# Kernel optimization log

Measured on AMD Instinct MI355X. Metric: run time of the kernel, lower is better.

Reference implementation:

```python
import jax, jax.numpy as jnp
import numpy as np

B, L, E, DK = 16, 2048, 1024, 128
MODE = "Decoder"


def setup_inputs() -> dict:
    key = jax.random.key(0)
    ks = jax.random.split(key, 6)
    x = jax.random.normal(ks[0], (B, L, E), dtype=jnp.float32)
    context = jax.random.normal(ks[1], (B, L, E), dtype=jnp.float32)
    batch_lengths = jax.random.randint(ks[2], (B,), 1, L + 1)  # valid lengths in [1, L]
    Wq = jax.random.normal(ks[3], (E, DK), dtype=jnp.float32) * 0.02
    Wk = jax.random.normal(ks[4], (E, DK), dtype=jnp.float32) * 0.02
    Wv = jax.random.normal(ks[5], (E, DK), dtype=jnp.float32) * 0.02
    return {"x": x, "context": context, "batch_lengths": batch_lengths,
            "Wq": Wq, "Wk": Wk, "Wv": Wv, "max_len": L}


def reference(x, context, batch_lengths, Wq, Wk, Wv, max_len):
    # x, context: [B, L, E]; batch_lengths: [B] ints; weights: [E, DK]
    Lq = x.shape[1]
    dk = Wq.shape[1]
    pos = jnp.arange(Lq)
    # outputMask: zero out padded time steps, broadcast over feature dim [B, L, 1]
    len_mask = (pos[None, :] < batch_lengths[:, None]).astype(x.dtype)[:, :, None]
    Q = (context @ Wq) * len_mask
    K = (context @ Wk) * len_mask
    V = (x @ Wv) * len_mask
    # energy: [B, Lq, Lk]
    energy = jnp.einsum("bqd,bkd->bqk", Q, K)
    # attnMask: -inf on padded key positions
    key_valid = pos[None, None, :] < batch_lengths[:, None, None]  # [B,1,Lk]
    if MODE == "Decoder":
        causal = pos[None, :, None] >= pos[None, None, :]  # j <= i
        key_valid = key_valid & causal
    energy = jnp.where(key_valid, energy, -jnp.inf)
    score = jax.nn.softmax(energy / jnp.sqrt(jnp.asarray(dk, x.dtype)), axis=-1)
    return jnp.einsum("bqk,bkd->bqd", score, V)
```

## Files before the change

### kernel.cpp

```cpp
#include <hip/hip_runtime.h>

#define DEV __device__ __forceinline__

typedef __attribute__((ext_vector_type(4))) float f32x4;
typedef __attribute__((ext_vector_type(4))) unsigned short u16x4;
typedef __attribute__((ext_vector_type(8))) __bf16 bf16x8;

constexpr int NB = 16, SL = 2048, EM = 1024, DKD = 128;

DEV unsigned short f2bf(float f) {
  unsigned int u = __float_as_uint(f);
  u += 0x7FFFu + ((u >> 16) & 1u);
  return (unsigned short)(u >> 16);
}

DEV f32x4 mfma16(bf16x8 a, bf16x8 b, f32x4 c) {
  return __builtin_amdgcn_mfma_f32_16x16x32_bf16(a, b, c, 0, 0, 0);
}

DEV void dma16(const void* g, void* l) {
  __builtin_amdgcn_global_load_lds(
      (const __attribute__((address_space(1))) unsigned int*)g,
      (__attribute__((address_space(3))) unsigned int*)l, 16, 0, 0);
}

DEV bf16x8 cvt8(f32x4 a, f32x4 b) {
  bf16x8 r;
  r[0] = (__bf16)a[0]; r[1] = (__bf16)a[1]; r[2] = (__bf16)a[2]; r[3] = (__bf16)a[3];
  r[4] = (__bf16)b[0]; r[5] = (__bf16)b[1]; r[6] = (__bf16)b[2]; r[7] = (__bf16)b[3];
  return r;
}

#define SBAR() __builtin_amdgcn_sched_barrier(0)

__global__ __launch_bounds__(256) void prep_w(
    const float* __restrict__ Wq, const float* __restrict__ Wk,
    const float* __restrict__ Wv, unsigned short* __restrict__ Wt,
    float* __restrict__ mvg)
{
  __shared__ unsigned short T[64 * 128];
  const int tid = threadIdx.x;
  if (blockIdx.x == 0) {
    #pragma unroll
    for (int i = 0; i < NB * DKD / 256; ++i) mvg[i * 256 + tid] = 0.f;
  }
  const int m = blockIdx.x >> 4, kc = blockIdx.x & 15;
  const float* W = (m == 0) ? Wq : ((m == 1) ? Wk : Wv);
  #pragma unroll
  for (int it = 0; it < 8; ++it) {
    int idx = it * 256 + tid;
    int kk = idx >> 5, n4 = (idx & 31) * 4;
    f32x4 w4 = *(const f32x4*)(W + (size_t)(kc * 64 + kk) * DKD + n4);
    *(u16x4*)&T[kk * 128 + n4] =
        u16x4{ f2bf(w4[0]), f2bf(w4[1]), f2bf(w4[2]), f2bf(w4[3]) };
  }
  __syncthreads();
  #pragma unroll
  for (int it = 0; it < 4; ++it) {
    int idx = it * 256 + tid;
    int p = idx & 7, n = idx >> 3;
    int c = p ^ (n & 7);
    unsigned short v[8];
    #pragma unroll
    for (int e = 0; e < 8; ++e) v[e] = T[(c * 8 + e) * 128 + n];
    size_t t = ((size_t)(m * 16 + kc) * 128 + n) * 8 + p;
    *(u16x4*)(Wt + t * 8)     = u16x4{v[0], v[1], v[2], v[3]};
    *(u16x4*)(Wt + t * 8 + 4) = u16x4{v[4], v[5], v[6], v[7]};
  }
}

__global__ __launch_bounds__(256, 2) void proj_qk(
    const float* __restrict__ ctx, const unsigned short* __restrict__ Wt,
    const int* __restrict__ lens, unsigned short* __restrict__ Qo,
    unsigned short* __restrict__ Kz)
{
  __shared__ float Als[2][64 * 64];
  const int tid = threadIdx.x;
  const int wave = tid >> 6, lane = tid & 63;
  const int quad = lane >> 4, mm = lane & 15;
  const int rb = blockIdx.x * 64;
  const int len = lens[blockIdx.x >> 5];
  if ((rb & (SL - 1)) >= len) return;

  f32x4 acc[4][4];
  #pragma unroll
  for (int i = 0; i < 4; ++i)
    #pragma unroll
    for (int j = 0; j < 4; ++j) acc[i][j] = f32x4{0.f, 0.f, 0.f, 0.f};

  const float* asrc[4];
  #pragma unroll
  for (int i = 0; i < 4; ++i) {
    const int rl_ = wave * 16 + i * 4 + (lane >> 4);
    const int cc  = (lane & 8) | ((lane & 7) ^ (rl_ & 7));
    asrc[i] = ctx + (size_t)(rb + rl_) * EM + cc * 4;
  }
  int soff[2][2];
  #pragma unroll
  for (int ks = 0; ks < 2; ++ks) {
    soff[ks][0] = (ks * 8 + ((quad * 2)     ^ (mm & 7))) * 4;
    soff[ks][1] = (ks * 8 + ((quad * 2 + 1) ^ (mm & 7))) * 4;
  }
  const unsigned short* bbase[4][2];
  #pragma unroll
  for (int lo = 0; lo < 4; ++lo)
    #pragma unroll
    for (int ks = 0; ks < 2; ++ks) {
      const int nrow = (wave * 4 + lo) * 16 + mm;
      const int pp = (ks * 4 + quad) ^ (mm & 7);
      const int cs = nrow * 8 + pp;
      bbase[lo][ks] = Wt + ((size_t)(cs >> 10) * 16384 + (cs & 1023)) * 8;
    }

  #pragma unroll
  for (int i = 0; i < 4; ++i)
    dma16(asrc[i],      (char*)Als[0] + wave * 4096 + i * 1024);
  #pragma unroll
  for (int i = 0; i < 4; ++i)
    dma16(asrc[i] + 64, (char*)Als[1] + wave * 4096 + i * 1024);
  __asm__ volatile("s_waitcnt vmcnt(4)" ::: "memory");
  __builtin_amdgcn_s_barrier();

  #pragma unroll 1
  for (int kc = 0; kc < 16; ++kc) {
    SBAR();
    bf16x8 bfr[4][2];
    #pragma unroll
    for (int lo = 0; lo < 4; ++lo)
      #pragma unroll
      for (int ks = 0; ks < 2; ++ks)
        bfr[lo][ks] = *(const bf16x8*)(bbase[lo][ks] + (size_t)kc * 8192);
    bf16x8 af[4][2];
    #pragma unroll
    for (int rt = 0; rt < 4; ++rt) {
      const float* rbase = Als[kc & 1] + (rt * 16 + mm) * 64;
      #pragma unroll
      for (int ks = 0; ks < 2; ++ks) {
        f32x4 a0 = *(const f32x4*)(rbase + soff[ks][0]);
        f32x4 a1 = *(const f32x4*)(rbase + soff[ks][1]);
        af[rt][ks] = cvt8(a0, a1);
      }
    }
    __asm__ volatile("s_waitcnt lgkmcnt(0)" ::: "memory");
    SBAR();
    __builtin_amdgcn_s_barrier();
    {
      const int kn = (kc + 2 < 16) ? (kc + 2) : 15;
      #pragma unroll
      for (int i = 0; i < 4; ++i)
        dma16(asrc[i] + kn * 64, (char*)Als[kc & 1] + wave * 4096 + i * 1024);
    }
    #pragma unroll
    for (int lo = 0; lo < 4; ++lo)
      #pragma unroll
      for (int ks = 0; ks < 2; ++ks)
        #pragma unroll
        for (int rt = 0; rt < 4; ++rt)
          acc[rt][lo] = mfma16(af[rt][ks], bfr[lo][ks], acc[rt][lo]);
    __builtin_amdgcn_s_barrier();
  }
  __asm__ volatile("s_waitcnt vmcnt(0)" ::: "memory");

  const float SCALE = 1.4426950408889634f * 0.08838834764831845f;
  #pragma unroll
  for (int rt = 0; rt < 4; ++rt)
    #pragma unroll
    for (int lo = 0; lo < 4; ++lo) {
      const int ctg = wave * 4 + lo;
      #pragma unroll
      for (int reg = 0; reg < 4; ++reg) {
        const int row = rb + rt * 16 + quad * 4 + reg;
        const int j = row & (SL - 1);
        const float val = acc[rt][lo][reg];
        if (ctg < 8) {
          const int d = ctg * 16 + mm;
          Qo[(size_t)row * DKD + d] = f2bf(val * ((j < len) ? SCALE : 0.f));
        } else {
          const int d = (ctg - 8) * 16 + mm;
          Kz[(size_t)row * DKD + (((d >> 3) ^ (j & 15)) * 8) + (d & 7)] = f2bf(val);
        }
      }
    }
}

__global__ __launch_bounds__(256, 2) void proj_v(
    const float* __restrict__ x, const unsigned short* __restrict__ Wt,
    const int* __restrict__ lens, unsigned short* __restrict__ Vz,
    float* __restrict__ mvg)
{
  __shared__ float Als[2][64 * 64];
  const int tid = threadIdx.x;
  const int wave = tid >> 6, lane = tid & 63;
  const int quad = lane >> 4, mm = lane & 15;
  const int rb = blockIdx.x * 64;
  const int bidx = blockIdx.x >> 5;
  const int len = lens[bidx];
  if ((rb & (SL - 1)) >= len) return;

  f32x4 acc[4][2];
  #pragma unroll
  for (int i = 0; i < 4; ++i) { acc[i][0] = f32x4{0.f,0.f,0.f,0.f}; acc[i][1] = f32x4{0.f,0.f,0.f,0.f}; }

  const float* asrc[4];
  #pragma unroll
  for (int i = 0; i < 4; ++i) {
    const int rl_ = wave * 16 + i * 4 + (lane >> 4);
    const int cc  = (lane & 8) | ((lane & 7) ^ (rl_ & 7));
    asrc[i] = x + (size_t)(rb + rl_) * EM + cc * 4;
  }
  int soff[2][2];
  #pragma unroll
  for (int ks = 0; ks < 2; ++ks) {
    soff[ks][0] = (ks * 8 + ((quad * 2)     ^ (mm & 7))) * 4;
    soff[ks][1] = (ks * 8 + ((quad * 2 + 1) ^ (mm & 7))) * 4;
  }
  const unsigned short* bbase[2][2];
  #pragma unroll
  for (int lo = 0; lo < 2; ++lo)
    #pragma unroll
    for (int ks = 0; ks < 2; ++ks) {
      const int nrow = (wave * 2 + lo) * 16 + mm;
      const int pp = (ks * 4 + quad) ^ (mm & 7);
      const int cs = nrow * 8 + pp;
      bbase[lo][ks] = Wt + ((size_t)2 * 16384 + cs) * 8;
    }

  #pragma unroll
  for (int i = 0; i < 4; ++i)
    dma16(asrc[i],      (char*)Als[0] + wave * 4096 + i * 1024);
  #pragma unroll
  for (int i = 0; i < 4; ++i)
    dma16(asrc[i] + 64, (char*)Als[1] + wave * 4096 + i * 1024);
  __asm__ volatile("s_waitcnt vmcnt(4)" ::: "memory");
  __builtin_amdgcn_s_barrier();

  #pragma unroll 1
  for (int kc = 0; kc < 16; ++kc) {
    SBAR();
    bf16x8 bfr[2][2];
    #pragma unroll
    for (int lo = 0; lo < 2; ++lo)
      #pragma unroll
      for (int ks = 0; ks < 2; ++ks)
        bfr[lo][ks] = *(const bf16x8*)(bbase[lo][ks] + (size_t)kc * 8192);
    bf16x8 af[4][2];
    #pragma unroll
    for (int rt = 0; rt < 4; ++rt) {
      const float* rbase = Als[kc & 1] + (rt * 16 + mm) * 64;
      #pragma unroll
      for (int ks = 0; ks < 2; ++ks) {
        f32x4 a0 = *(const f32x4*)(rbase + soff[ks][0]);
        f32x4 a1 = *(const f32x4*)(rbase + soff[ks][1]);
        af[rt][ks] = cvt8(a0, a1);
      }
    }
    __asm__ volatile("s_waitcnt lgkmcnt(0)" ::: "memory");
    SBAR();
    __builtin_amdgcn_s_barrier();
    {
      const int kn = (kc + 2 < 16) ? (kc + 2) : 15;
      #pragma unroll
      for (int i = 0; i < 4; ++i)
        dma16(asrc[i] + kn * 64, (char*)Als[kc & 1] + wave * 4096 + i * 1024);
    }
    #pragma unroll
    for (int lo = 0; lo < 2; ++lo)
      #pragma unroll
      for (int ks = 0; ks < 2; ++ks)
        #pragma unroll
        for (int rt = 0; rt < 4; ++rt)
          acc[rt][lo] = mfma16(af[rt][ks], bfr[lo][ks], acc[rt][lo]);
    __builtin_amdgcn_s_barrier();
  }
  __asm__ volatile("s_waitcnt vmcnt(0)" ::: "memory");

  #pragma unroll
  for (int rt = 0; rt < 4; ++rt)
    #pragma unroll
    for (int lo = 0; lo < 2; ++lo) {
      const int d = (wave * 2 + lo) * 16 + mm;
      const int row0 = rb + rt * 16 + quad * 4;
      const int b = row0 >> 11, j0 = row0 & (SL - 1);
      u16x4 pk = u16x4{ f2bf(acc[rt][lo][0]), f2bf(acc[rt][lo][1]),
                        f2bf(acc[rt][lo][2]), f2bf(acc[rt][lo][3]) };
      size_t off = (size_t)b * DKD * SL + (size_t)d * SL + (j0 & ~63)
                 + ((((j0 >> 3) & 7) ^ (d & 7)) * 8) + (j0 & 7);
      *(u16x4*)(Vz + off) = pk;
    }

  const int jb = rb & (SL - 1);
  #pragma unroll
  for (int lo = 0; lo < 2; ++lo) {
    const int d = (wave * 2 + lo) * 16 + mm;
    float part = 0.f;
    #pragma unroll
    for (int rt = 0; rt < 4; ++rt) {
      const int jr = jb + rt * 16 + quad * 4;
      #pragma unroll
      for (int reg = 0; reg < 4; ++reg)
        if (jr + reg < len) part += acc[rt][lo][reg];
    }
    part += __shfl_xor(part, 16);
    part += __shfl_xor(part, 32);
    if (quad == 0) atomicAdd(mvg + bidx * DKD + d, part);
  }
}

__global__ __launch_bounds__(256, 2) void attn(
    const unsigned short* __restrict__ Qw, const unsigned short* __restrict__ Kz,
    const unsigned short* __restrict__ Vz, const float* __restrict__ mvg,
    const int* __restrict__ lens, float* __restrict__ out)
{
  __shared__ unsigned short Ks[2][64 * 128];
  __shared__ unsigned short Vs[2][128 * 64];
  __shared__ unsigned short Ps[4][16 * 72];
  const int tid = threadIdx.x;
  const int wave = tid >> 6, lane = tid & 63;
  const int quad = lane >> 4, mm = lane & 15;
  const int b = blockIdx.y;
  const int qb = ((int)gridDim.x - 1 - (int)blockIdx.x) * 64;
  const int len = lens[b];

  if (qb >= len) {
    const int dd = (tid & 31) * 4;
    const int r0 = tid >> 5;
    const f32x4 m4 = *(const f32x4*)(mvg + b * DKD + dd);
    const float inv = 1.0f / (float)len;
    const f32x4 val = f32x4{ m4[0]*inv, m4[1]*inv, m4[2]*inv, m4[3]*inv };
    #pragma unroll
    for (int it = 0; it < 8; ++it) {
      const int row = qb + it * 8 + r0;
      *(f32x4*)(out + ((size_t)b * SL + row) * DKD + dd) = val;
    }
    return;
  }

  const int kend = min(qb + 64, len);
  const int nblk = (kend + 63) >> 6;
  const int irow0 = qb + wave * 16 + quad * 4;

  bf16x8 aQ[4];
  {
    const unsigned short* qbase =
        Qw + (size_t)(b * SL + qb + wave * 16 + mm) * DKD + quad * 8;
    #pragma unroll
    for (int cc = 0; cc < 4; ++cc) aQ[cc] = *(const bf16x8*)(qbase + cc * 32);
  }
  bf16x8 onesb;
  #pragma unroll
  for (int i = 0; i < 8; ++i) onesb[i] = (__bf16)1.0f;

  float mr[4];
  #pragma unroll
  for (int r = 0; r < 4; ++r) mr[r] = -__builtin_inff();
  f32x4 acc[8];
  #pragma unroll
  for (int i = 0; i < 8; ++i) acc[i] = f32x4{0.f,0.f,0.f,0.f};
  f32x4 accl = f32x4{0.f,0.f,0.f,0.f};

  #pragma unroll
  for (int it = 0; it < 4; ++it) {
    int s = it * 256 + tid;
    dma16(Kz + (size_t)(b * SL) * DKD + (size_t)s * 8,
          (char*)Ks[0] + (it * 256 + wave * 64) * 16);
  }
  #pragma unroll
  for (int it = 0; it < 4; ++it) {
    int s = it * 256 + tid;
    int d = s >> 3, p = s & 7;
    dma16(Vz + (size_t)b * DKD * SL + (size_t)d * SL + p * 8,
          (char*)Vs[0] + (it * 256 + wave * 64) * 16);
  }

  #pragma unroll 1
  for (int blk = 0; blk < nblk; ++blk) {
    const int kb = blk * 64;
    __syncthreads();
    if (blk + 1 < nblk) {
      const int kb1 = kb + 64;
      const int nb = (blk + 1) & 1;
      #pragma unroll
      for (int it = 0; it < 4; ++it) {
        int s = it * 256 + tid;
        dma16(Kz + (size_t)(b * SL + kb1) * DKD + (size_t)s * 8,
              (char*)Ks[nb] + (it * 256 + wave * 64) * 16);
      }
      #pragma unroll
      for (int it = 0; it < 4; ++it) {
        int s = it * 256 + tid;
        int d = s >> 3, p = s & 7;
        dma16(Vz + (size_t)b * DKD * SL + (size_t)d * SL + kb1 + p * 8,
              (char*)Vs[nb] + (it * 256 + wave * 64) * 16);
      }
    }
    const unsigned short* kbuf = Ks[blk & 1];
    const unsigned short* vbuf = Vs[blk & 1];

    f32x4 s4[4];
    #pragma unroll
    for (int nt = 0; nt < 4; ++nt) {
      f32x4 c = f32x4{0.f,0.f,0.f,0.f};
      const int j = nt * 16 + mm;
      #pragma unroll
      for (int cc = 0; cc < 4; ++cc) {
        const int pp = (cc * 4 + quad) ^ mm;
        bf16x8 kf = *(const bf16x8*)(kbuf + j * 128 + pp * 8);
        c = mfma16(aQ[cc], kf, c);
      }
      s4[nt] = c;
    }

    float alpha[4];
    #pragma unroll
    for (int reg = 0; reg < 4; ++reg) {
      const int jl = min(irow0 + reg + 1, len);
      float v0 = (kb + mm      < jl) ? s4[0][reg] : -__builtin_inff();
      float v1 = (kb + 16 + mm < jl) ? s4[1][reg] : -__builtin_inff();
      float v2 = (kb + 32 + mm < jl) ? s4[2][reg] : -__builtin_inff();
      float v3 = (kb + 48 + mm < jl) ? s4[3][reg] : -__builtin_inff();
      float mx = fmaxf(fmaxf(v0, v1), fmaxf(v2, v3));
      #pragma unroll
      for (int xm = 1; xm < 16; xm <<= 1) mx = fmaxf(mx, __shfl_xor(mx, xm));
      const float mn = fmaxf(mr[reg], mx);
      alpha[reg] = __builtin_amdgcn_exp2f(mr[reg] - mn);
      const float p0 = __builtin_amdgcn_exp2f(v0 - mn);
      const float p1 = __builtin_amdgcn_exp2f(v1 - mn);
      const float p2 = __builtin_amdgcn_exp2f(v2 - mn);
      const float p3 = __builtin_amdgcn_exp2f(v3 - mn);
      mr[reg] = mn;
      const int prow = quad * 4 + reg;
      Ps[wave][prow * 72 + mm]      = f2bf(p0);
      Ps[wave][prow * 72 + 16 + mm] = f2bf(p1);
      Ps[wave][prow * 72 + 32 + mm] = f2bf(p2);
      Ps[wave][prow * 72 + 48 + mm] = f2bf(p3);
    }
    #pragma unroll
    for (int nt = 0; nt < 8; ++nt) {
      f32x4 a = acc[nt];
      a[0] *= alpha[0]; a[1] *= alpha[1]; a[2] *= alpha[2]; a[3] *= alpha[3];
      acc[nt] = a;
    }
    accl[0] *= alpha[0]; accl[1] *= alpha[1];
    accl[2] *= alpha[2]; accl[3] *= alpha[3];
    __asm__ volatile("s_waitcnt lgkmcnt(0)" ::: "memory");
    bf16x8 aP[2];
    #pragma unroll
    for (int ks = 0; ks < 2; ++ks)
      aP[ks] = *(const bf16x8*)(&Ps[wave][mm * 72 + ks * 32 + quad * 8]);
    #pragma unroll
    for (int ks = 0; ks < 2; ++ks) {
      #pragma unroll
      for (int nt = 0; nt < 8; ++nt) {
        const int pp = (ks * 4 + quad) ^ (mm & 7);
        bf16x8 vf = *(const bf16x8*)(vbuf + (nt * 16 + mm) * 64 + pp * 8);
        acc[nt] = mfma16(aP[ks], vf, acc[nt]);
      }
      accl = mfma16(aP[ks], onesb, accl);
    }
  }

  #pragma unroll
  for (int reg = 0; reg < 4; ++reg) {
    const float rl = 1.0f / accl[reg];
    const size_t base = ((size_t)b * SL + irow0 + reg) * DKD + mm;
    #pragma unroll
    for (int nt = 0; nt < 8; ++nt)
      out[base + nt * 16] = acc[nt][reg] * rl;
  }
}

extern "C" void kernel_launch(void* const* d_in, const int* in_sizes, int n_in,
                              void* d_out, int out_size, void* d_ws, size_t ws_size,
                              hipStream_t stream) {
  const float* x    = (const float*)d_in[0];
  const float* ctx  = (const float*)d_in[1];
  const int*   lens = (const int*)d_in[2];
  const float* Wq   = (const float*)d_in[3];
  const float* Wk   = (const float*)d_in[4];
  const float* Wv   = (const float*)d_in[5];
  float* out = (float*)d_out;

  const size_t QKV = (size_t)NB * SL * DKD * sizeof(unsigned short);
  const size_t WTSZ = (size_t)3 * 16 * 128 * 8 * 8 * sizeof(unsigned short);
  const size_t MVSZ = (size_t)NB * DKD * sizeof(float);
  if (ws_size < 3 * QKV + WTSZ + MVSZ) return;
  unsigned short* Qws = (unsigned short*)d_ws;
  unsigned short* Kzs = (unsigned short*)((char*)d_ws + QKV);
  unsigned short* Vzs = (unsigned short*)((char*)d_ws + 2 * QKV);
  unsigned short* Wt  = (unsigned short*)((char*)d_ws + 3 * QKV);
  float*          mvg = (float*)((char*)d_ws + 3 * QKV + WTSZ);

  prep_w <<<dim3(48), 256, 0, stream>>>(Wq, Wk, Wv, Wt, mvg);
  proj_qk<<<dim3(NB * SL / 64), 256, 0, stream>>>(ctx, Wt, lens, Qws, Kzs);
  proj_v <<<dim3(NB * SL / 64), 256, 0, stream>>>(x, Wt, lens, Vzs, mvg);
  attn   <<<dim3(SL / 64, NB), 256, 0, stream>>>(Qws, Kzs, Vzs, mvg, lens, out);
}
```

Before: 346.8 us.

## Deepen projection GEMM pipeline to four LDS stages with register-prefetched weights

The Q/K and V projection kernels move from a two-stage to a four-stage LDS ring for activations and unroll the k-loop by two. Weight fragments are double-buffered in registers and prefetched one step ahead instead of being loaded just before use. This halves the number of barriers per k-chunk and hides more global latency behind MFMA work. The cost is doubled LDS (64KB per block), which may reduce occupancy at launch_bounds(256,2). Separately, the attention kernel raises wave priority around its MFMA blocks with s_setprio.

```diff
diff --git a/kernel.cpp b/kernel.cpp
--- a/kernel.cpp
+++ b/kernel.cpp
@@ -74,7 +74,7 @@
     const int* __restrict__ lens, unsigned short* __restrict__ Qo,
     unsigned short* __restrict__ Kz)
 {
-  __shared__ float Als[2][64 * 64];
+  __shared__ float Als[4][64 * 64];
   const int tid = threadIdx.x;
   const int wave = tid >> 6, lane = tid & 63;
   const int quad = lane >> 4, mm = lane & 15;
@@ -113,51 +113,95 @@
     }
 
   #pragma unroll
-  for (int i = 0; i < 4; ++i)
-    dma16(asrc[i],      (char*)Als[0] + wave * 4096 + i * 1024);
-  #pragma unroll
-  for (int i = 0; i < 4; ++i)
-    dma16(asrc[i] + 64, (char*)Als[1] + wave * 4096 + i * 1024);
-  __asm__ volatile("s_waitcnt vmcnt(4)" ::: "memory");
+  for (int i = 0; i < 4; ++i) dma16(asrc[i],       (char*)Als[0] + wave * 4096 + i * 1024);
+  #pragma unroll
+  for (int i = 0; i < 4; ++i) dma16(asrc[i] + 64,  (char*)Als[1] + wave * 4096 + i * 1024);
+  SBAR();
+  bf16x8 bA[4][2], bB[4][2];
+  #pragma unroll
+  for (int lo = 0; lo < 4; ++lo)
+    #pragma unroll
+    for (int ks = 0; ks < 2; ++ks) {
+      bA[lo][ks] = *(const bf16x8*)(bbase[lo][ks]);
+      bB[lo][ks] = *(const bf16x8*)(bbase[lo][ks] + 8192);
+    }
+  SBAR();
+  #pragma unroll
+  for (int i = 0; i < 4; ++i) dma16(asrc[i] + 128, (char*)Als[2] + wave * 4096 + i * 1024);
+  #pragma unroll
+  for (int i = 0; i < 4; ++i) dma16(asrc[i] + 192, (char*)Als[3] + wave * 4096 + i * 1024);
+  SBAR();
+  __asm__ volatile("s_waitcnt vmcnt(24)" ::: "memory");
   __builtin_amdgcn_s_barrier();
+  SBAR();
 
   #pragma unroll 1
-  for (int kc = 0; kc < 16; ++kc) {
-    SBAR();
-    bf16x8 bfr[4][2];
+  for (int s = 0; s < 8; ++s) {
+    const int kc0 = 2 * s, kc1 = 2 * s + 1;
+    bf16x8 af0[4][2];
+    #pragma unroll
+    for (int rt = 0; rt < 4; ++rt) {
+      const float* rbase = Als[kc0 & 3] + (rt * 16 + mm) * 64;
+      #pragma unroll
+      for (int ks = 0; ks < 2; ++ks)
+        af0[rt][ks] = cvt8(*(const f32x4*)(rbase + soff[ks][0]),
+                           *(const f32x4*)(rbase + soff[ks][1]));
+    }
     #pragma unroll
     for (int lo = 0; lo < 4; ++lo)
       #pragma unroll
       for (int ks = 0; ks < 2; ++ks)
-        bfr[lo][ks] = *(const bf16x8*)(bbase[lo][ks] + (size_t)kc * 8192);
-    bf16x8 af[4][2];
+        #pragma unroll
+        for (int rt = 0; rt < 4; ++rt)
+          acc[rt][lo] = mfma16(af0[rt][ks], bA[lo][ks], acc[rt][lo]);
+    {
+      const int kn = (kc0 + 2 < 16) ? (kc0 + 2) : 15;
+      #pragma unroll
+      for (int lo = 0; lo < 4; ++lo)
+        #pragma unroll
+        for (int ks = 0; ks < 2; ++ks)
+          bA[lo][ks] = *(const bf16x8*)(bbase[lo][ks] + (size_t)kn * 8192);
+    }
+    bf16x8 af1[4][2];
     #pragma unroll
     for (int rt = 0; rt < 4; ++rt) {
-      const float* rbase = Als[kc & 1] + (rt * 16 + mm) * 64;
-      #pragma unroll
-      for (int ks = 0; ks < 2; ++ks) {
-        f32x4 a0 = *(const f32x4*)(rbase + soff[ks][0]);
-        f32x4 a1 = *(const f32x4*)(rbase + soff[ks][1]);
-        af[rt][ks] = cvt8(a0, a1);
-      }
+      const float* rbase = Als[kc1 & 3] + (rt * 16 + mm) * 64;
+      #pragma unroll
+      for (int ks = 0; ks < 2; ++ks)
+        af1[rt][ks] = cvt8(*(const f32x4*)(rbase + soff[ks][0]),
+                           *(const f32x4*)(rbase + soff[ks][1]));
+    }
+    #pragma unroll
+    for (int lo = 0; lo < 4; ++lo)
+      #pragma unroll
+      for (int ks = 0; ks < 2; ++ks)
+        #pragma unroll
+        for (int rt = 0; rt < 4; ++rt)
+          acc[rt][lo] = mfma16(af1[rt][ks], bB[lo][ks], acc[rt][lo]);
+    {
+      const int kn = (kc0 + 3 < 16) ? (kc0 + 3) : 15;
+      #pragma unroll
+      for (int lo = 0; lo < 4; ++lo)
+        #pragma unroll
+        for (int ks = 0; ks < 2; ++ks)
+          bB[lo][ks] = *(const bf16x8*)(bbase[lo][ks] + (size_t)kn * 8192);
     }
     __asm__ volatile("s_waitcnt lgkmcnt(0)" ::: "memory");
     SBAR();
     __builtin_amdgcn_s_barrier();
     {
-      const int kn = (kc + 2 < 16) ? (kc + 2) : 15;
+      const int k4 = (kc0 + 4 < 16) ? (kc0 + 4) : 15;
+      const int k5 = (kc0 + 5 < 16) ? (kc0 + 5) : 15;
       #pragma unroll
       for (int i = 0; i < 4; ++i)
-        dma16(asrc[i] + kn * 64, (char*)Als[kc & 1] + wave * 4096 + i * 1024);
-    }
-    #pragma unroll
-    for (int lo = 0; lo < 4; ++lo)
-      #pragma unroll
-      for (int ks = 0; ks < 2; ++ks)
-        #pragma unroll
-        for (int rt = 0; rt < 4; ++rt)
-          acc[rt][lo] = mfma16(af[rt][ks], bfr[lo][ks], acc[rt][lo]);
+        dma16(asrc[i] + k4 * 64, (char*)Als[kc0 & 3] + wave * 4096 + i * 1024);
+      #pragma unroll
+      for (int i = 0; i < 4; ++i)
+        dma16(asrc[i] + k5 * 64, (char*)Als[kc1 & 3] + wave * 4096 + i * 1024);
+    }
+    __asm__ volatile("s_waitcnt vmcnt(24)" ::: "memory");
     __builtin_amdgcn_s_barrier();
+    SBAR();
   }
   __asm__ volatile("s_waitcnt vmcnt(0)" ::: "memory");
 
@@ -188,7 +232,7 @@
     const int* __restrict__ lens, unsigned short* __restrict__ Vz,
     float* __restrict__ mvg)
 {
-  __shared__ float Als[2][64 * 64];
+  __shared__ float Als[4][64 * 64];
   const int tid = threadIdx.x;
   const int wave = tid >> 6, lane = tid & 63;
   const int quad = lane >> 4, mm = lane & 15;
@@ -226,51 +270,95 @@
     }
 
   #pragma unroll
-  for (int i = 0; i < 4; ++i)
-    dma16(asrc[i],      (char*)Als[0] + wave * 4096 + i * 1024);
-  #pragma unroll
-  for (int i = 0; i < 4; ++i)
-    dma16(asrc[i] + 64, (char*)Als[1] + wave * 4096 + i * 1024);
-  __asm__ volatile("s_waitcnt vmcnt(4)" ::: "memory");
+  for (int i = 0; i < 4; ++i) dma16(asrc[i],       (char*)Als[0] + wave * 4096 + i * 1024);
+  #pragma unroll
+  for (int i = 0; i < 4; ++i) dma16(asrc[i] + 64,  (char*)Als[1] + wave * 4096 + i * 1024);
+  SBAR();
+  bf16x8 bA[2][2], bB[2][2];
+  #pragma unroll
+  for (int lo = 0; lo < 2; ++lo)
+    #pragma unroll
+    for (int ks = 0; ks < 2; ++ks) {
+      bA[lo][ks] = *(const bf16x8*)(bbase[lo][ks]);
+      bB[lo][ks] = *(const bf16x8*)(bbase[lo][ks] + 8192);
+    }
+  SBAR();
+  #pragma unroll
+  for (int i = 0; i < 4; ++i) dma16(asrc[i] + 128, (char*)Als[2] + wave * 4096 + i * 1024);
+  #pragma unroll
+  for (int i = 0; i < 4; ++i) dma16(asrc[i] + 192, (char*)Als[3] + wave * 4096 + i * 1024);
+  SBAR();
+  __asm__ volatile("s_waitcnt vmcnt(16)" ::: "memory");
   __builtin_amdgcn_s_barrier();
+  SBAR();
 
   #pragma unroll 1
-  for (int kc = 0; kc < 16; ++kc) {
-    SBAR();
-    bf16x8 bfr[2][2];
+  for (int s = 0; s < 8; ++s) {
+    const int kc0 = 2 * s, kc1 = 2 * s + 1;
+    bf16x8 af0[4][2];
+    #pragma unroll
+    for (int rt = 0; rt < 4; ++rt) {
+      const float* rbase = Als[kc0 & 3] + (rt * 16 + mm) * 64;
+      #pragma unroll
+      for (int ks = 0; ks < 2; ++ks)
+        af0[rt][ks] = cvt8(*(const f32x4*)(rbase + soff[ks][0]),
+                           *(const f32x4*)(rbase + soff[ks][1]));
+    }
     #pragma unroll
     for (int lo = 0; lo < 2; ++lo)
       #pragma unroll
       for (int ks = 0; ks < 2; ++ks)
-        bfr[lo][ks] = *(const bf16x8*)(bbase[lo][ks] + (size_t)kc * 8192);
-    bf16x8 af[4][2];
+        #pragma unroll
+        for (int rt = 0; rt < 4; ++rt)
+          acc[rt][lo] = mfma16(af0[rt][ks], bA[lo][ks], acc[rt][lo]);
+    {
+      const int kn = (kc0 + 2 < 16) ? (kc0 + 2) : 15;
+      #pragma unroll
+      for (int lo = 0; lo < 2; ++lo)
+        #pragma unroll
+        for (int ks = 0; ks < 2; ++ks)
+          bA[lo][ks] = *(const bf16x8*)(bbase[lo][ks] + (size_t)kn * 8192);
+    }
+    bf16x8 af1[4][2];
     #pragma unroll
     for (int rt = 0; rt < 4; ++rt) {
-      const float* rbase = Als[kc & 1] + (rt * 16 + mm) * 64;
-      #pragma unroll
-      for (int ks = 0; ks < 2; ++ks) {
-        f32x4 a0 = *(const f32x4*)(rbase + soff[ks][0]);
-        f32x4 a1 = *(const f32x4*)(rbase + soff[ks][1]);
-        af[rt][ks] = cvt8(a0, a1);
-      }
+      const float* rbase = Als[kc1 & 3] + (rt * 16 + mm) * 64;
+      #pragma unroll
+      for (int ks = 0; ks < 2; ++ks)
+        af1[rt][ks] = cvt8(*(const f32x4*)(rbase + soff[ks][0]),
+                           *(const f32x4*)(rbase + soff[ks][1]));
+    }
+    #pragma unroll
+    for (int lo = 0; lo < 2; ++lo)
+      #pragma unroll
+      for (int ks = 0; ks < 2; ++ks)
+        #pragma unroll
+        for (int rt = 0; rt < 4; ++rt)
+          acc[rt][lo] = mfma16(af1[rt][ks], bB[lo][ks], acc[rt][lo]);
+    {
+      const int kn = (kc0 + 3 < 16) ? (kc0 + 3) : 15;
+      #pragma unroll
+      for (int lo = 0; lo < 2; ++lo)
+        #pragma unroll
+        for (int ks = 0; ks < 2; ++ks)
+          bB[lo][ks] = *(const bf16x8*)(bbase[lo][ks] + (size_t)kn * 8192);
     }
     __asm__ volatile("s_waitcnt lgkmcnt(0)" ::: "memory");
     SBAR();
     __builtin_amdgcn_s_barrier();
     {
-      const int kn = (kc + 2 < 16) ? (kc + 2) : 15;
+      const int k4 = (kc0 + 4 < 16) ? (kc0 + 4) : 15;
+      const int k5 = (kc0 + 5 < 16) ? (kc0 + 5) : 15;
       #pragma unroll
       for (int i = 0; i < 4; ++i)
-        dma16(asrc[i] + kn * 64, (char*)Als[kc & 1] + wave * 4096 + i * 1024);
-    }
-    #pragma unroll
-    for (int lo = 0; lo < 2; ++lo)
-      #pragma unroll
-      for (int ks = 0; ks < 2; ++ks)
-        #pragma unroll
-        for (int rt = 0; rt < 4; ++rt)
-          acc[rt][lo] = mfma16(af[rt][ks], bfr[lo][ks], acc[rt][lo]);
+        dma16(asrc[i] + k4 * 64, (char*)Als[kc0 & 3] + wave * 4096 + i * 1024);
+      #pragma unroll
+      for (int i = 0; i < 4; ++i)
+        dma16(asrc[i] + k5 * 64, (char*)Als[kc1 & 3] + wave * 4096 + i * 1024);
+    }
+    __asm__ volatile("s_waitcnt vmcnt(16)" ::: "memory");
     __builtin_amdgcn_s_barrier();
+    SBAR();
   }
   __asm__ volatile("s_waitcnt vmcnt(0)" ::: "memory");
 
@@ -397,6 +485,7 @@
     const unsigned short* vbuf = Vs[blk & 1];
 
     f32x4 s4[4];
+    __builtin_amdgcn_s_setprio(1);
     #pragma unroll
     for (int nt = 0; nt < 4; ++nt) {
       f32x4 c = f32x4{0.f,0.f,0.f,0.f};
@@ -409,6 +498,7 @@
       }
       s4[nt] = c;
     }
+    __builtin_amdgcn_s_setprio(0);
 
     float alpha[4];
     #pragma unroll
@@ -447,6 +537,7 @@
     #pragma unroll
     for (int ks = 0; ks < 2; ++ks)
       aP[ks] = *(const bf16x8*)(&Ps[wave][mm * 72 + ks * 32 + quad * 8]);
+    __builtin_amdgcn_s_setprio(1);
     #pragma unroll
     for (int ks = 0; ks < 2; ++ks) {
       #pragma unroll
@@ -457,6 +548,7 @@
       }
       accl = mfma16(aP[ks], onesb, accl);
     }
+    __builtin_amdgcn_s_setprio(0);
   }
 
   #pragma unroll
```

Measured after the change: 348.4 us. About the same (+0.5%).
